# Performance work log

Measured on AMD Instinct MI355X. Metric: run time of the kernel, lower is better.

The kernel has to match this reference:

```python
import jax, jax.numpy as jnp
import numpy as np

SIGMA = 1.0
DELTA = 1.0
TOPK = 10
TOPK_HALF = 5  # int(np.around(TOPK / 2))
N, D = 4096, 512
N_IDS = 2048  # N / view


def _l2_normalize(x, eps=1e-12):
    n = jnp.linalg.norm(x, axis=1, keepdims=True)
    return x / jnp.maximum(n, eps)


def _cdist(a, b):
    # Euclidean distance with a sqrt that is safe at 0 (diagonal).
    sq = (jnp.sum(a * a, 1)[:, None] + jnp.sum(b * b, 1)[None, :]
          - 2.0 * (a @ b.T))
    sq = jnp.maximum(sq, 0.0)
    return jnp.where(sq > 0, jnp.sqrt(jnp.where(sq > 0, sq, 1.0)), 0.0)


def setup_inputs() -> dict:
    key = jax.random.key(0)
    k1, k2, k3 = jax.random.split(key, 3)
    s_emb = jax.random.normal(k1, (N, D), dtype=jnp.float32)
    t_emb = jax.random.normal(k2, (N, D), dtype=jnp.float32)
    idx = jax.random.randint(k3, (N,), 0, N_IDS, dtype=jnp.int64)
    return {"s_emb": s_emb, "t_emb": t_emb, "idx": idx}


def reference(s_emb, t_emb, idx):
    n = s_emb.shape[0]
    s = _l2_normalize(s_emb)          # disable_mu=True
    t = _l2_normalize(t_emb)

    S_dist = _cdist(s, s)
    S_dist = S_dist / jnp.mean(S_dist, axis=1, keepdims=True)

    # --- teacher-side neighbor graph (no_grad in original) ---
    T_dist = _cdist(t, t)
    W_P = jnp.exp(-(T_dist ** 2) / SIGMA)                      # [N,N]
    same = idx[:, None] == idx[None, :]
    W_P_copy = jnp.where(same, 1.0, W_P)
    _, topk_index = jax.lax.top_k(W_P_copy, TOPK)              # [N,k]
    topk_half_index = topk_index[:, :TOPK_HALF]                # [N,k/2]

    rows = jnp.arange(n)[:, None]
    W_NN = jnp.zeros((n, n), jnp.float32).at[rows, topk_index].set(1.0)
    V = ((W_NN + W_NN.T) / 2.0 == 1.0).astype(jnp.float32)     # mutual kNN

    # Vectorized form of the per-row nonzero gather-reduce loop:
    # W_C_tilda[i,j] = V[i,j] * (sum_l V[i,l] V[j,l]) / |{l: V[i,l]>0}|
    row_cnt = jnp.sum(V, axis=1)                               # [N]
    VV = jnp.einsum('il,jl->ij', V, V)                         # [N,N]
    W_C_tilda = jnp.where(V > 0, VV / jnp.maximum(row_cnt, 1.0)[:, None], 0.0)

    W_C_hat = jnp.mean(W_C_tilda[topk_half_index], axis=1)     # [N,k/2,N]->[N,N]
    W_C = (W_C_hat + W_C_hat.T) / 2.0
    W = (W_P + W_C) / 2.0

    eye = jnp.eye(n, dtype=jnp.float32)
    pos_weight = W * (1.0 - eye)
    neg_weight = (1.0 - W) * (1.0 - eye)

    pull = jnp.maximum(S_dist, 0.0) ** 2 * pos_weight
    push = jnp.maximum(DELTA - S_dist, 0.0) ** 2 * neg_weight
    loss = (jnp.sum(pull) + jnp.sum(push)) / (n * (n - 1))
    return loss
```

## Files before the change

### kernel.cpp

```cpp
#include <hip/hip_runtime.h>
#include <math.h>

#define N 4096
#define D 512
#define TOPK 10
#define TOPK_HALF 5
#define NT 32
#define TRI_BLOCKS (NT * (NT + 1) / 2)
#define WC_BLOCKS (N * TOPK_HALF / 16)
#define INV_N (1.0f / 4096.0f)
#define TPAD 132

typedef __bf16 bf16;
typedef __bf16 bf16x4 __attribute__((ext_vector_type(4)));
typedef __bf16 bf16x8 __attribute__((ext_vector_type(8)));
typedef float f32x4 __attribute__((ext_vector_type(4)));
typedef _Float16 f16;
typedef _Float16 f16x4 __attribute__((ext_vector_type(4)));
typedef _Float16 f16x8 __attribute__((ext_vector_type(8)));
typedef unsigned short u16;
typedef unsigned short u16x8 __attribute__((ext_vector_type(8)));
typedef unsigned int u32;

__device__ __forceinline__ void gl_lds16(const void* g, void* l) {
  __builtin_amdgcn_global_load_lds(
      (const __attribute__((address_space(1))) void*)g,
      (__attribute__((address_space(3))) void*)l, 16, 0, 0);
}

__device__ __forceinline__ float f16tof(u16 h) {
  return (float)__builtin_bit_cast(_Float16, h);
}

__global__ __launch_bounds__(256) void k_normalize2(const float* __restrict__ xs,
                                                    const float* __restrict__ xt,
                                                    bf16* __restrict__ ys,
                                                    bf16* __restrict__ yt,
                                                    float* __restrict__ rsq_s,
                                                    float* __restrict__ rsq_t,
                                                    float* __restrict__ rowsum) {
  int b = blockIdx.x;
  int tid = threadIdx.x;
  int half = tid >> 7;
  int l = tid & 127;
  int row2 = 2 * b + half;
  int is_t = row2 >> 12;
  int row = row2 & (N - 1);
  const float* x = is_t ? xt : xs;
  bf16* y = is_t ? yt : ys;
  float* rowsq = is_t ? rsq_t : rsq_s;
  const float* xr = x + (size_t)row * D;
  float4 v = *(const float4*)(xr + l * 4);
  float ss = v.x * v.x + v.y * v.y + v.z * v.z + v.w * v.w;
  __shared__ float red[4];
  __shared__ float red2[4];
  for (int off = 32; off > 0; off >>= 1) ss += __shfl_down(ss, off, 64);
  if ((tid & 63) == 0) red[tid >> 6] = ss;
  __syncthreads();
  float tot = red[half * 2] + red[half * 2 + 1];
  float inv = 1.0f / fmaxf(sqrtf(tot), 1e-12f);
  bf16x4 bv;
  bv[0] = (bf16)(v.x * inv); bv[1] = (bf16)(v.y * inv);
  bv[2] = (bf16)(v.z * inv); bv[3] = (bf16)(v.w * inv);
  *(bf16x4*)(y + (size_t)row * D + l * 4) = bv;
  float f0 = (float)bv[0], f1 = (float)bv[1], f2 = (float)bv[2], f3 = (float)bv[3];
  float s2 = f0 * f0 + f1 * f1 + f2 * f2 + f3 * f3;
  for (int off = 32; off > 0; off >>= 1) s2 += __shfl_down(s2, off, 64);
  if ((tid & 63) == 0) red2[tid >> 6] = s2;
  __syncthreads();
  if ((tid & 127) == 0) {
    rowsq[row] = red2[half * 2] + red2[half * 2 + 1];
    if (!is_t) rowsum[row] = 0.f;
  }
}

__global__ __launch_bounds__(256) void k_dgram3(const bf16* __restrict__ S,
                                                const bf16* __restrict__ T,
                                                const float* __restrict__ rsq_s,
                                                const float* __restrict__ rsq_t,
                                                f16* __restrict__ Gsd,
                                                f16* __restrict__ Gwp,
                                                float* __restrict__ rowsum) {
  __shared__ __align__(16) char sm[49152];
  f16* tp = (f16*)sm;

  int z = blockIdx.y;
  const bf16* Y = z ? T : S;
  const float* rsq = z ? rsq_t : rsq_s;
  f16* G = z ? Gwp : Gsd;

  int orig = blockIdx.x;
  int t = (orig & 7) * (TRI_BLOCKS / 8) + (orig >> 3);
  int by = 0;
  while (t >= NT - by) { t -= NT - by; ++by; }
  int bx = by + t;
  bool offdiag = (bx != by);

  int tid = threadIdx.x;
  int lane = tid & 63, w = tid >> 6;
  int wr = w >> 1, wc = w & 1;
  int quad = lane >> 4, c = lane & 15;
  int w1024 = w << 10;

  const char* Jbase = (const char*)(Y + (size_t)(bx * 128) * D);
  const char* Ibase = (const char*)(Y + (size_t)(by * 128) * D);
  int r0 = tid >> 2, q0 = tid & 3;
  int r1 = (tid + 256) >> 2, q1 = (tid + 256) & 3;
  size_t so0 = (size_t)r0 * (D * 2) + q0 * 16;
  size_t so1 = (size_t)r1 * (D * 2) + q1 * 16;

  int jrow = wr * 64 + c;
  int irow = wc * 64 + c;
  int kq = quad * 8;

#define STAGE(buf, kb)                                   \
  {                                                      \
    char* _b = (buf);                                    \
    gl_lds16(Jbase + so0 + (kb), _b + w1024);            \
    gl_lds16(Jbase + so1 + (kb), _b + 4096 + w1024);     \
    gl_lds16(Ibase + so0 + (kb), _b + 8192 + w1024);     \
    gl_lds16(Ibase + so1 + (kb), _b + 12288 + w1024);    \
  }

#define COMPUTE(bufc)                                                          \
  {                                                                            \
    const bf16* Jc = (const bf16*)(bufc);                                      \
    const bf16* Ic = (const bf16*)((bufc) + 8192);                             \
    bf16x8 af[4], bfr[4];                                                      \
    _Pragma("unroll") for (int u = 0; u < 4; ++u)                              \
        af[u] = *(const bf16x8*)&Jc[(jrow + u * 16) * 32 + kq];                \
    _Pragma("unroll") for (int v = 0; v < 4; ++v)                              \
        bfr[v] = *(const bf16x8*)&Ic[(irow + v * 16) * 32 + kq];               \
    _Pragma("unroll") for (int u = 0; u < 4; ++u)                              \
      _Pragma("unroll") for (int v = 0; v < 4; ++v)                            \
        acc[u][v] = __builtin_amdgcn_mfma_f32_16x16x32_bf16(                   \
            af[u], bfr[v], acc[u][v], 0, 0, 0);                                \
  }

  f32x4 acc[4][4] = {};
  STAGE(sm, 0);
  STAGE(sm + 16384, 64);
  int sc = 0, sn = 2;
  for (int tt = 0; tt < 14; ++tt) {
    char* nb = sm + (sn << 14);
    asm volatile("s_barrier" ::: "memory");
    STAGE(nb, (size_t)(tt + 2) * 64);
    asm volatile("s_waitcnt vmcnt(8)\n\ts_barrier" ::: "memory");
    COMPUTE(sm + (sc << 14));
    sc = (sc == 2) ? 0 : sc + 1;
    sn = (sn == 2) ? 0 : sn + 1;
  }
  asm volatile("s_waitcnt vmcnt(4)\n\ts_barrier" ::: "memory");
  COMPUTE(sm + 32768);
  asm volatile("s_waitcnt vmcnt(0)\n\ts_barrier" ::: "memory");
  COMPUTE(sm);
  __syncthreads();

#undef STAGE
#undef COMPUTE

#pragma unroll
  for (int v = 0; v < 4; ++v) {
    int il = wc * 64 + v * 16 + c;
    int ig = by * 128 + il;
    float ri = rsq[ig];
    float rsv = 0.f;
#pragma unroll
    for (int u = 0; u < 4; ++u) {
      int jl0 = wr * 64 + u * 16 + quad * 4;
      int jb0i = bx * 128 + jl0;
      float4 rj = *(const float4*)(rsq + jb0i);
      const float* rjp = (const float*)&rj;
      f32x4 a = acc[u][v];
      f16x4 st;
      if (z == 0) {
#pragma unroll
        for (int reg = 0; reg < 4; ++reg) {
          float sq = fmaxf(ri + rjp[reg] - 2.0f * a[reg], 0.0f);
          float val = __builtin_amdgcn_sqrtf(sq);
          st[reg] = (_Float16)val;
          rsv += val;
        }
      } else {
#pragma unroll
        for (int reg = 0; reg < 4; ++reg) {
          float sq = fmaxf(ri + rjp[reg] - 2.0f * a[reg], 0.0f);
          st[reg] = (_Float16)__expf(-sq);
        }
      }
      *(f16x4*)(G + (size_t)ig * N + jb0i) = st;
      if (offdiag) {
#pragma unroll
        for (int reg = 0; reg < 4; ++reg) tp[(jl0 + reg) * TPAD + il] = st[reg];
      }
    }
    if (z == 0) {
      rsv += __shfl_xor(rsv, 16, 64);
      rsv += __shfl_xor(rsv, 32, 64);
      if (lane < 16) atomicAdd(&rowsum[ig], rsv);
    }
  }

  if (offdiag) {
    __syncthreads();
    int rloc = tid >> 4;
    int cseg = tid & 15;
#pragma unroll
    for (int it = 0; it < 8; ++it) {
      int jl = it * 16 + rloc;
      int jg = bx * 128 + jl;
      f16x8 v8 = *(f16x8*)&tp[jl * TPAD + cseg * 8];
      *(f16x8*)(G + (size_t)jg * N + by * 128 + cseg * 8) = v8;
      if (z == 0) {
        float csum = 0.f;
#pragma unroll
        for (int e = 0; e < 8; ++e) csum += (float)v8[e];
        csum += __shfl_xor(csum, 1, 64);
        csum += __shfl_xor(csum, 2, 64);
        csum += __shfl_xor(csum, 4, 64);
        csum += __shfl_xor(csum, 8, 64);
        if (cseg == 0) atomicAdd(&rowsum[jg], csum);
      }
    }
  }
}

__global__ __launch_bounds__(256) void k_rowpass(const f16* __restrict__ Gs,
                                                 const f16* __restrict__ Gw,
                                                 const int* __restrict__ ids,
                                                 const float* __restrict__ rowsum,
                                                 int* __restrict__ topk,
                                                 double* __restrict__ pd) {
  __shared__ u32 lds[256 * TOPK];
  __shared__ double dred[4];
  int i = blockIdx.x, tid = threadIdx.x;
  int idi = ids[i];
  float invm = 1.0f / (rowsum[i] * INV_N);
  const u16* srow = (const u16*)(Gs + (size_t)i * N);
  const u16* wrow = (const u16*)(Gw + (size_t)i * N);
  u32 key[16];
  float dsum = 0.f;
  int j0 = tid * 16;
#pragma unroll
  for (int h = 0; h < 2; ++h) {
    int jb = j0 + h * 8;
    u16x8 sv = *(const u16x8*)(srow + jb);
    u16x8 wv = *(const u16x8*)(wrow + jb);
    int4 id0 = *(const int4*)(ids + jb);
    int4 id1 = *(const int4*)(ids + jb + 4);
    const int* idp = (const int*)&id0;
    const int* idp1 = (const int*)&id1;
#pragma unroll
    for (int e = 0; e < 8; ++e) {
      int j = jb + e;
      u16 hw = wv[e];
      float wp = f16tof(hw);
      if (j != i) {
        float sdn = f16tof(sv[e]) * invm;
        float r = fmaxf(1.0f - sdn, 0.0f); r *= r;
        dsum += r + 0.5f * wp * (sdn * sdn - r);
      }
      int idj = (e < 4) ? idp[e] : idp1[e - 4];
      u16 hk = (idj == idi) ? (u16)0x3C00 : hw;
      key[h * 8 + e] = ((u32)hk << 16) | (u32)(4095 - j);
    }
  }
#pragma unroll
  for (int kk = 2; kk <= 16; kk <<= 1) {
#pragma unroll
    for (int jj = kk >> 1; jj > 0; jj >>= 1) {
#pragma unroll
      for (int ii = 0; ii < 16; ++ii) {
        int ll = ii ^ jj;
        if (ll > ii) {
          bool desc = ((ii & kk) == 0);
          u32 a = key[ii], b = key[ll];
          bool sw = desc ? (a < b) : (a > b);
          key[ii] = sw ? b : a;
          key[ll] = sw ? a : b;
        }
      }
    }
  }
  double dl = (double)dsum;
  for (int off = 32; off > 0; off >>= 1) dl += __shfl_down(dl, off, 64);
  if ((tid & 63) == 0) dred[tid >> 6] = dl;
#pragma unroll
  for (int o = 0; o < TOPK; ++o) lds[tid * TOPK + o] = key[o];
  __syncthreads();
  for (int off = 128; off >= 1; off >>= 1) {
    if (tid < off) {
      u32 A[TOPK], B[TOPK];
#pragma unroll
      for (int o = 0; o < TOPK; ++o) {
        A[o] = lds[tid * TOPK + o];
        B[o] = lds[(tid + off) * TOPK + o];
      }
      u32 out[TOPK];
#pragma unroll
      for (int o = 0; o < TOPK; ++o) {
        u32 m = A[o] > B[o] ? A[o] : B[o];
#pragma unroll
        for (int p = 0; p < o; ++p) {
          u32 mn = A[p] < B[o - 1 - p] ? A[p] : B[o - 1 - p];
          m = m > mn ? m : mn;
        }
        out[o] = m;
      }
#pragma unroll
      for (int o = 0; o < TOPK; ++o) lds[tid * TOPK + o] = out[o];
    }
    __syncthreads();
  }
  if (tid == 0) {
#pragma unroll
    for (int o = 0; o < TOPK; ++o)
      topk[i * TOPK + o] = 4095 - (int)(lds[o] & 0xFFFu);
    pd[i] = dred[0] + dred[1] + dred[2] + dred[3];
  }
}

__global__ __launch_bounds__(256) void k_buildV(const int* __restrict__ topk,
                                                int* __restrict__ L,
                                                int* __restrict__ cnt) {
  int tid = threadIdx.x;
  int grp = tid >> 4, gl = tid & 15;
  int i = blockIdx.x * 16 + grp;
  bool act = (gl < TOPK);
  int j = act ? topk[i * TOPK + gl] : 0;
  bool mut = false;
  if (act) {
#pragma unroll
    for (int q = 0; q < TOPK; ++q) mut |= (topk[j * TOPK + q] == i);
  }
  unsigned long long m = __ballot(mut);
  int base = tid & 48;
  unsigned gm = (unsigned)((m >> base) & 0xFFFFull);
  int pos = __popc(gm & ((1u << gl) - 1));
  if (mut) L[i * TOPK + pos] = j;
  if (gl == 0) cnt[i] = __popc(gm);
}

__global__ __launch_bounds__(256) void k_wc(const int* __restrict__ topk,
                                            const int* __restrict__ L,
                                            const int* __restrict__ cnt,
                                            const f16* __restrict__ Gsd,
                                            const float* __restrict__ rowsum,
                                            double* __restrict__ pw) {
  __shared__ double red[16];
  int tid = threadIdx.x;
  int grp = tid >> 4;
  int gl = tid & 15;
  int task = blockIdx.x * 16 + grp;
  int i = task / TOPK_HALF, m = task % TOPK_HALF;
  int r = topk[i * TOPK + m];
  int cr = cnt[r];
  float invmi = 1.0f / (rowsum[i] * INV_N);
  int lval = (gl < cr) ? L[r * TOPK + gl] : -1;
  int Lr[TOPK];
#pragma unroll
  for (int a = 0; a < TOPK; ++a) Lr[a] = __shfl(lval, a, 16);
  float contrib = 0.f;
  if (gl < cr) {
    int j = lval;
    if (j != i) {
      int cj = cnt[j];
      float mj = rowsum[j] * INV_N;
      float sr_ = f16tof(((const u16*)Gsd)[(size_t)i * N + j]);
      int lj[TOPK];
#pragma unroll
      for (int b = 0; b < TOPK; ++b) lj[b] = L[j * TOPK + b];
      int vv = 0;
#pragma unroll
      for (int b = 0; b < TOPK; ++b) {
        if (b < cj) {
#pragma unroll
          for (int a = 0; a < TOPK; ++a)
            vv += ((a < cr) && (lj[b] == Lr[a])) ? 1 : 0;
        }
      }
      float denom = (float)(cr > 1 ? cr : 1);
      float wgt = (float)vv / denom;
      float sdij = sr_ * invmi;
      float sdji = sr_ / mj;
      float Rij = fmaxf(1.0f - sdij, 0.0f); Rij *= Rij;
      float Rji = fmaxf(1.0f - sdji, 0.0f); Rji *= Rji;
      float Fij = sdij * sdij - Rij;
      float Fji = sdji * sdji - Rji;
      contrib = wgt * (Fij + Fji);
    }
  }
  double local = (double)contrib;
  local += __shfl_xor(local, 1, 16);
  local += __shfl_xor(local, 2, 16);
  local += __shfl_xor(local, 4, 16);
  local += __shfl_xor(local, 8, 16);
  if (gl == 0) red[grp] = local;
  __syncthreads();
  if (tid == 0) {
    double s = 0.0;
#pragma unroll
    for (int g = 0; g < 16; ++g) s += red[g];
    pw[blockIdx.x] = s * (1.0 / 20.0);
  }
}

__global__ __launch_bounds__(256) void k_final(const double* __restrict__ pd,
                                               const double* __restrict__ pw,
                                               float* __restrict__ out) {
  int tid = threadIdx.x;
  double s = 0.0;
  for (int i = tid; i < N; i += 256) s += pd[i];
  for (int i = tid; i < WC_BLOCKS; i += 256) s += pw[i];
  for (int off = 32; off > 0; off >>= 1) s += __shfl_down(s, off, 64);
  __shared__ double red[4];
  if ((tid & 63) == 0) red[tid >> 6] = s;
  __syncthreads();
  if (tid == 0)
    out[0] = (float)((red[0] + red[1] + red[2] + red[3]) /
                     ((double)N * (double)(N - 1)));
}

extern "C" void kernel_launch(void* const* d_in, const int* in_sizes, int n_in,
                              void* d_out, int out_size, void* d_ws, size_t ws_size,
                              hipStream_t stream) {
  const float* s_emb = (const float*)d_in[0];
  const float* t_emb = (const float*)d_in[1];
  const int* ids = (const int*)d_in[2];
  float* out = (float*)d_out;

  char* ws = (char*)d_ws;
  size_t off = 0;
  bf16* snorm = (bf16*)(ws + off); off += (size_t)N * D * 2;
  bf16* tnorm = (bf16*)(ws + off); off += (size_t)N * D * 2;
  f16*  Gsd   = (f16*)(ws + off);  off += (size_t)N * N * 2;
  f16*  Gwp   = (f16*)(ws + off);  off += (size_t)N * N * 2;
  float* rsq_s = (float*)(ws + off); off += (size_t)N * 4;
  float* rsq_t = (float*)(ws + off); off += (size_t)N * 4;
  float* rowsum= (float*)(ws + off); off += (size_t)N * 4;
  int*   topk  = (int*)(ws + off);   off += (size_t)N * TOPK * 4;
  int*   L     = (int*)(ws + off);   off += (size_t)N * TOPK * 4;
  int*   cnt   = (int*)(ws + off);   off += (size_t)N * 4;
  off = (off + 15) & ~(size_t)15;
  double* pd   = (double*)(ws + off); off += (size_t)N * 8;
  double* pw   = (double*)(ws + off); off += (size_t)WC_BLOCKS * 8;

  k_normalize2<<<N, 256, 0, stream>>>(s_emb, t_emb, snorm, tnorm,
                                      rsq_s, rsq_t, rowsum);
  k_dgram3<<<dim3(TRI_BLOCKS, 2), 256, 0, stream>>>(snorm, tnorm, rsq_s, rsq_t,
                                                    Gsd, Gwp, rowsum);
  k_rowpass<<<N, 256, 0, stream>>>(Gsd, Gwp, ids, rowsum, topk, pd);
  k_buildV<<<N / 16, 256, 0, stream>>>(topk, L, cnt);
  k_wc<<<WC_BLOCKS, 256, 0, stream>>>(topk, L, cnt, Gsd, rowsum, pw);
  k_final<<<1, 256, 0, stream>>>(pd, pw, out);
}
```

Measured before the change: 145.7 us.

## Replace triple-buffered K=32 pipeline with single-buffer K=64 XOR-swizzled staging

Rewrites the Gram-matrix main loop to stage 64-wide K chunks (8 iterations instead of 16) into a single LDS buffer using an XOR swizzle on 16-byte columns, which is meant to cut LDS bank conflicts on fragment reads. It drops the triple-buffered prefetch and its offset vmcnt waits, shrinking LDS from 48KB to 33KB and allowing more resident blocks. In exchange, global loads are no longer overlapped with MFMA work inside a block. Each iteration now waits for all loads and then hits a full barrier.

After: 154.0 us. 1.06x slower.

```diff
diff --git a/kernel.cpp b/kernel.cpp
--- a/kernel.cpp
+++ b/kernel.cpp
@@ -81,7 +81,7 @@
                                                 f16* __restrict__ Gsd,
                                                 f16* __restrict__ Gwp,
                                                 float* __restrict__ rowsum) {
-  __shared__ __align__(16) char sm[49152];
+  __shared__ __align__(16) char sm[33792];
   f16* tp = (f16*)sm;
 
   int z = blockIdx.y;
@@ -100,64 +100,58 @@
   int lane = tid & 63, w = tid >> 6;
   int wr = w >> 1, wc = w & 1;
   int quad = lane >> 4, c = lane & 15;
-  int w1024 = w << 10;
 
   const char* Jbase = (const char*)(Y + (size_t)(bx * 128) * D);
   const char* Ibase = (const char*)(Y + (size_t)(by * 128) * D);
-  int r0 = tid >> 2, q0 = tid & 3;
-  int r1 = (tid + 256) >> 2, q1 = (tid + 256) & 3;
-  size_t so0 = (size_t)r0 * (D * 2) + q0 * 16;
-  size_t so1 = (size_t)r1 * (D * 2) + q1 * 16;
+
+  int goff[4];
+  int ldso[4];
+#pragma unroll
+  for (int i = 0; i < 4; ++i) {
+    int s = i * 256 + tid;
+    int r = s >> 3;
+    int cs = (tid & 7) ^ (r & 7);
+    goff[i] = r * (D * 2) + cs * 16;
+    ldso[i] = (i * 256 + w * 64) * 16;
+  }
 
   int jrow = wr * 64 + c;
   int irow = wc * 64 + c;
-  int kq = quad * 8;
-
-#define STAGE(buf, kb)                                   \
-  {                                                      \
-    char* _b = (buf);                                    \
-    gl_lds16(Jbase + so0 + (kb), _b + w1024);            \
-    gl_lds16(Jbase + so1 + (kb), _b + 4096 + w1024);     \
-    gl_lds16(Ibase + so0 + (kb), _b + 8192 + w1024);     \
-    gl_lds16(Ibase + so1 + (kb), _b + 12288 + w1024);    \
-  }
-
-#define COMPUTE(bufc)                                                          \
-  {                                                                            \
-    const bf16* Jc = (const bf16*)(bufc);                                      \
-    const bf16* Ic = (const bf16*)((bufc) + 8192);                             \
-    bf16x8 af[4], bfr[4];                                                      \
-    _Pragma("unroll") for (int u = 0; u < 4; ++u)                              \
-        af[u] = *(const bf16x8*)&Jc[(jrow + u * 16) * 32 + kq];                \
-    _Pragma("unroll") for (int v = 0; v < 4; ++v)                              \
-        bfr[v] = *(const bf16x8*)&Ic[(irow + v * 16) * 32 + kq];               \
-    _Pragma("unroll") for (int u = 0; u < 4; ++u)                              \
-      _Pragma("unroll") for (int v = 0; v < 4; ++v)                            \
-        acc[u][v] = __builtin_amdgcn_mfma_f32_16x16x32_bf16(                   \
-            af[u], bfr[v], acc[u][v], 0, 0, 0);                                \
-  }
+  int x7 = c & 7;
+  int csx0 = ((quad) ^ x7) * 16;
+  int csx1 = ((4 + quad) ^ x7) * 16;
 
   f32x4 acc[4][4] = {};
-  STAGE(sm, 0);
-  STAGE(sm + 16384, 64);
-  int sc = 0, sn = 2;
-  for (int tt = 0; tt < 14; ++tt) {
-    char* nb = sm + (sn << 14);
-    asm volatile("s_barrier" ::: "memory");
-    STAGE(nb, (size_t)(tt + 2) * 64);
-    asm volatile("s_waitcnt vmcnt(8)\n\ts_barrier" ::: "memory");
-    COMPUTE(sm + (sc << 14));
-    sc = (sc == 2) ? 0 : sc + 1;
-    sn = (sn == 2) ? 0 : sn + 1;
-  }
-  asm volatile("s_waitcnt vmcnt(4)\n\ts_barrier" ::: "memory");
-  COMPUTE(sm + 32768);
-  asm volatile("s_waitcnt vmcnt(0)\n\ts_barrier" ::: "memory");
-  COMPUTE(sm);
-  __syncthreads();
-
-#undef STAGE
-#undef COMPUTE
+  for (int tt = 0; tt < 8; ++tt) {
+    int kb = tt * 128;
+#pragma unroll
+    for (int i = 0; i < 4; ++i) gl_lds16(Jbase + goff[i] + kb, sm + ldso[i]);
+#pragma unroll
+    for (int i = 0; i < 4; ++i) gl_lds16(Ibase + goff[i] + kb, sm + 16384 + ldso[i]);
+    asm volatile("s_waitcnt vmcnt(0)\n\ts_barrier" ::: "memory");
+    {
+      const char* Jc = sm;
+      const char* Ic = sm + 16384;
+#pragma unroll
+      for (int m = 0; m < 2; ++m) {
+        int csx = m ? csx1 : csx0;
+        bf16x8 af[4], bfr[4];
+#pragma unroll
+        for (int u = 0; u < 4; ++u)
+          af[u] = *(const bf16x8*)(Jc + jrow * 128 + u * 2048 + csx);
+#pragma unroll
+        for (int v = 0; v < 4; ++v)
+          bfr[v] = *(const bf16x8*)(Ic + irow * 128 + v * 2048 + csx);
+#pragma unroll
+        for (int u = 0; u < 4; ++u)
+#pragma unroll
+          for (int v = 0; v < 4; ++v)
+            acc[u][v] = __builtin_amdgcn_mfma_f32_16x16x32_bf16(
+                af[u], bfr[v], acc[u][v], 0, 0, 0);
+      }
+    }
+    asm volatile("s_waitcnt lgkmcnt(0)\n\ts_barrier" ::: "memory");
+  }
 
 #pragma unroll
   for (int v = 0; v < 4; ++v) {
```
